# Kernel tuning notes

Measured on AMD Instinct MI355X. Metric: run time of the kernel, lower is better.

Reference implementation:

```python
import jax, jax.numpy as jnp
import numpy as np

B, F, D = 16384, 32, 64
EPS = 1e-5


def layer_norm(x, g, b):
    m = x.mean(-1, keepdims=True)
    v = ((x - m) ** 2).mean(-1, keepdims=True)
    return (x - m) / jnp.sqrt(v + EPS) * g + b


def setup_inputs() -> dict:
    key = jax.random.key(0)
    ks = jax.random.split(key, 24)
    IN = F * D

    def w(k, shape, fan_in):
        return jax.random.normal(k, shape, dtype=jnp.float32) / np.sqrt(fan_in)

    return {
        "x": jax.random.normal(ks[0], (B, F, D), dtype=jnp.float32),
        # StaticGRN (mask branch): Linear(IN,D) -> ELU -> Linear(D,F); skip Linear(IN,F); GateAndNorm(F)
        "mw1": w(ks[1], (IN, D), IN), "mb1": jnp.zeros((D,), jnp.float32),
        "mw2": w(ks[2], (D, F), D), "mb2": jnp.zeros((F,), jnp.float32),
        "mlw": w(ks[3], (IN, F), IN), "mlb": jnp.zeros((F,), jnp.float32),
        "mgw": w(ks[4], (F, F), F), "mgb": jnp.zeros((F,), jnp.float32),
        "mlw2": w(ks[5], (F, F), F), "mlb2": jnp.zeros((F,), jnp.float32),
        "mgamma": jnp.ones((F,), jnp.float32), "mbeta": jnp.zeros((F,), jnp.float32),
        # Per-feature GRNNoContext params, stacked over F (batched small GEMMs)
        "w1": w(ks[6], (F, D, D), D), "b1": jnp.zeros((F, D), jnp.float32),
        "w2": w(ks[7], (F, D, D), D), "b2": jnp.zeros((F, D), jnp.float32),
        "gw": w(ks[8], (F, D, D), D), "gb": jnp.zeros((F, D), jnp.float32),
        "lw": w(ks[9], (F, D, D), D), "lb": jnp.zeros((F, D), jnp.float32),
        "gamma": jnp.ones((F, D), jnp.float32), "beta": jnp.zeros((F, D), jnp.float32),
    }


def reference(x, mw1, mb1, mw2, mb2, mlw, mlb, mgw, mgb, mlw2, mlb2, mgamma, mbeta,
              w1, b1, w2, b2, gw, gb, lw, lb, gamma, beta):
    b, f, d = x.shape
    flat = x.reshape(b, f * d)
    # StaticGRN mask branch (dropout is 0.0 -> identity)
    h = jax.nn.elu(flat @ mw1 + mb1) @ mw2 + mb2          # [B,F]
    res = flat @ mlw + mlb                                 # [B,F] skip path
    pre = jax.nn.sigmoid(h @ mgw + mgb) * (h @ mlw2 + mlb2) + res
    mask = jax.nn.softmax(layer_norm(pre, mgamma, mbeta), axis=-1)[:, None, :]  # [B,1,F]
    # Per-feature GRNs, batched over the feature axis
    hh = jax.nn.elu(jnp.einsum('bfd,fde->bfe', x, w1) + b1)
    hh = jnp.einsum('bfd,fde->bfe', hh, w2) + b2
    gate = jax.nn.sigmoid(jnp.einsum('bfd,fde->bfe', hh, gw) + gb)
    lin = jnp.einsum('bfd,fde->bfe', hh, lw) + lb
    vecs = layer_norm(gate * lin + x, gamma, beta)         # [B,F,D]
    out = jnp.einsum('bof,bfd->bod', mask, vecs)[:, 0, :]  # [B,D]
    return out, mask
```

## Files before the change

### kernel.cpp

```cpp
#include <hip/hip_runtime.h>
#include <hip/hip_bf16.h>
#include <math.h>

#define NB 16384
#define NF 32
#define ND 64
#define NIN 2048

typedef __attribute__((ext_vector_type(8))) short fragA;
typedef __attribute__((ext_vector_type(4))) float fragC;

#define MFMA(a, b, c) __builtin_amdgcn_mfma_f32_16x16x32_bf16((a), (b), (c), 0, 0, 0)

__device__ __forceinline__ short f2bf(float f) {
    union { float f; unsigned u; } v; v.f = f;
    return (short)((v.u + 0x7fffu + ((v.u >> 16) & 1u)) >> 16);
}
__device__ __forceinline__ fragA cvt8(const float* p) {
    const float4 a = *(const float4*)p;
    const float4 b = *(const float4*)(p + 4);
    union { __hip_bfloat162 h[4]; fragA f; } u;
    u.h[0] = __float22bfloat162_rn(make_float2(a.x, a.y));
    u.h[1] = __float22bfloat162_rn(make_float2(a.z, a.w));
    u.h[2] = __float22bfloat162_rn(make_float2(b.x, b.y));
    u.h[3] = __float22bfloat162_rn(make_float2(b.z, b.w));
    return u.f;
}

__global__ __launch_bounds__(256) void prep_kernel(
    const float* __restrict__ w1, const float* __restrict__ w2,
    const float* __restrict__ gw, const float* __restrict__ lw,
    const float* __restrict__ mw1, const float* __restrict__ mlw,
    const float* __restrict__ mw2, const float* __restrict__ mgw,
    const float* __restrict__ mlw2,
    short* __restrict__ wsout)
{
    int F = blockIdx.x * 256 + threadIdx.x;
    fragA o;
    if (F < 65536) {
        int mat = F >> 14;
        int f   = (F >> 9) & 31;
        int nt  = (F >> 7) & 3;
        int s   = (F >> 6) & 1;
        int l   = F & 63;
        const float* src = (mat == 0 ? w1 : mat == 1 ? w2 : mat == 2 ? gw : lw)
                           + (size_t)f * 4096;
        int n  = nt * 16 + (l & 15);
        int k0 = s * 32 + ((l >> 4) << 3);
#pragma unroll
        for (int j = 0; j < 8; ++j) o[j] = f2bf(src[(k0 + j) * 64 + n]);
    } else if (F < 90112) {
        int G  = F - 65536;
        int f  = G / 768;
        int r  = G - f * 768;
        int nt = r >> 7;
        int s  = (r >> 6) & 1;
        int l  = r & 63;
        int n  = nt * 16 + (l & 15);
        int k0 = f * 64 + s * 32 + ((l >> 4) << 3);
        if (n < 64) {
#pragma unroll
            for (int j = 0; j < 8; ++j) o[j] = f2bf(mw1[(size_t)(k0 + j) * 64 + n]);
        } else {
#pragma unroll
            for (int j = 0; j < 8; ++j) o[j] = f2bf(mlw[(size_t)(k0 + j) * 32 + (n - 64)]);
        }
    } else {
        int G2 = F - 90112;
        if (G2 < 256) {
            int nt = G2 >> 7, s = (G2 >> 6) & 1, l = G2 & 63;
            int n = nt * 16 + (l & 15);
            int k0 = s * 32 + ((l >> 4) << 3);
#pragma unroll
            for (int j = 0; j < 8; ++j) o[j] = f2bf(mw2[(k0 + j) * 32 + n]);
        } else {
            int G3 = G2 - 256;
            const float* src = (G3 < 128) ? mgw : mlw2;
            G3 &= 127;
            int nt = G3 >> 6, l = G3 & 63;
            int n = nt * 16 + (l & 15);
            int k0 = (l >> 4) << 3;
#pragma unroll
            for (int j = 0; j < 8; ++j) o[j] = f2bf(src[(k0 + j) * 32 + n]);
        }
    }
    ((fragA*)wsout)[F] = o;
}

__global__ __launch_bounds__(256, 4) void fused_kernel(
    const float* __restrict__ x,
    const short* __restrict__ wfrag, const short* __restrict__ mwfrag,
    const short* __restrict__ swfrag,
    const float* __restrict__ mb1, const float* __restrict__ mb2,
    const float* __restrict__ mlb, const float* __restrict__ mgb,
    const float* __restrict__ mlb2,
    const float* __restrict__ mgamma, const float* __restrict__ mbeta,
    const float* __restrict__ b1, const float* __restrict__ b2,
    const float* __restrict__ gb, const float* __restrict__ lb,
    const float* __restrict__ gamma, const float* __restrict__ beta,
    float* __restrict__ mask_out, float* __restrict__ out)
{
    __shared__ float smem[8960];
    float* redS  = smem;
    float* gS    = smem;
    float* lS    = smem + 768;
    float* hS1   = smem + 1552;
    float* resS  = smem + 2640;
    float* h2S   = smem + 3216;
    float* outS  = smem + 4352;
    float* maskS = smem + 8448;

    const int tid = threadIdx.x;
    const int w = tid >> 6, l = tid & 63;
    const int row0 = blockIdx.x * 16;
    const int m = l & 15, q = l >> 4;

    const fragA* wf  = (const fragA*)wfrag;
    const fragA* mwf = (const fragA*)mwfrag;
    const fragA* swf = (const fragA*)swfrag;

    for (int i = tid; i < 1552; i += 256) redS[i] = 0.f;
    __syncthreads();

    fragC acc[6];
#pragma unroll
    for (int nt = 0; nt < 6; ++nt) acc[nt] = (fragC){0.f, 0.f, 0.f, 0.f};

    const float* xpm = x + (size_t)(row0 + m) * NIN + q * 8;
    for (int fi = 0; fi < 8; ++fi) {
        int f = w * 8 + fi;
        const float* xp = xpm + f * ND;
        fragA a0 = cvt8(xp), a1 = cvt8(xp + 32);
        const size_t fb = (size_t)f * 768 + l;
#pragma unroll
        for (int nt = 0; nt < 6; ++nt) {
            acc[nt] = MFMA(a0, mwf[fb + nt * 128], acc[nt]);
            acc[nt] = MFMA(a1, mwf[fb + nt * 128 + 64], acc[nt]);
        }
    }
#pragma unroll
    for (int nt = 0; nt < 6; ++nt)
#pragma unroll
        for (int rg = 0; rg < 4; ++rg)
            atomicAdd(&redS[(q * 4 + rg) * 97 + nt * 16 + m], acc[nt][rg]);
    __syncthreads();

    {
        int r = tid & 15, cb = tid >> 4;
#pragma unroll
        for (int i = 0; i < 6; ++i) {
            int c = cb + i * 16;
            float s = redS[r * 97 + c];
            if (c < 64) {
                float v = s + mb1[c];
                hS1[r * 68 + c] = v > 0.f ? v : expm1f(v);
            } else {
                resS[r * 36 + (c - 64)] = s + mlb[c - 64];
            }
        }
    }
    __syncthreads();

    if (w < 2) {
        const float* ap = hS1 + m * 68 + q * 8;
        fragA a0 = cvt8(ap), a1 = cvt8(ap + 32);
        fragC c = {0.f, 0.f, 0.f, 0.f};
        c = MFMA(a0, swf[w * 128 + l], c);
        c = MFMA(a1, swf[w * 128 + 64 + l], c);
        float bv = mb2[w * 16 + m];
#pragma unroll
        for (int rg = 0; rg < 4; ++rg)
            h2S[(q * 4 + rg) * 36 + w * 16 + m] = c[rg] + bv;
    }
    __syncthreads();

    {
        int ntc = w & 1;
        int isl = w >> 1;
        fragA a = cvt8(h2S + m * 36 + q * 8);
        fragC c = {0.f, 0.f, 0.f, 0.f};
        c = MFMA(a, swf[256 + isl * 128 + ntc * 64 + l], c);
        float* dst = isl ? lS : gS;
#pragma unroll
        for (int rg = 0; rg < 4; ++rg)
            dst[(q * 4 + rg) * 36 + ntc * 16 + m] = c[rg];
    }
    __syncthreads();

    if (w == 0) {
        int r2 = l >> 2, c0 = (l & 3) * 8;
        float pre[8];
#pragma unroll
        for (int i = 0; i < 8; ++i) {
            int c = c0 + i;
            float gg = gS[r2 * 36 + c] + mgb[c];
            float ll = lS[r2 * 36 + c] + mlb2[c];
            pre[i] = ll / (1.f + expf(-gg)) + resS[r2 * 36 + c];
        }
        float s1 = 0.f;
#pragma unroll
        for (int i = 0; i < 8; ++i) s1 += pre[i];
        s1 += __shfl_xor(s1, 1); s1 += __shfl_xor(s1, 2);
        float mean = s1 * (1.f / 32.f);
        float s2 = 0.f;
#pragma unroll
        for (int i = 0; i < 8; ++i) { float d = pre[i] - mean; s2 += d * d; }
        s2 += __shfl_xor(s2, 1); s2 += __shfl_xor(s2, 2);
        float inv = rsqrtf(s2 * (1.f / 32.f) + 1e-5f);
        float ln[8]; float mx = -3.4e38f;
#pragma unroll
        for (int i = 0; i < 8; ++i) {
            ln[i] = (pre[i] - mean) * inv * mgamma[c0 + i] + mbeta[c0 + i];
            mx = fmaxf(mx, ln[i]);
        }
        mx = fmaxf(mx, __shfl_xor(mx, 1));
        mx = fmaxf(mx, __shfl_xor(mx, 2));
        float ssum = 0.f;
#pragma unroll
        for (int i = 0; i < 8; ++i) { ln[i] = expf(ln[i] - mx); ssum += ln[i]; }
        ssum += __shfl_xor(ssum, 1); ssum += __shfl_xor(ssum, 2);
        float rs = 1.f / ssum;
        float* mo = mask_out + (size_t)(row0 + r2) * 32 + c0;
        *(float4*)mo       = (float4){ln[0] * rs, ln[1] * rs, ln[2] * rs, ln[3] * rs};
        *(float4*)(mo + 4) = (float4){ln[4] * rs, ln[5] * rs, ln[6] * rs, ln[7] * rs};
#pragma unroll
        for (int i = 0; i < 8; ++i) maskS[r2 * 32 + c0 + i] = ln[i] * rs;
    }
    __syncthreads();

    float* hW = smem + w * 1088;

    fragC oac[4];
#pragma unroll
    for (int nt = 0; nt < 4; ++nt) oac[nt] = (fragC){0.f, 0.f, 0.f, 0.f};

    for (int fi = 0; fi < 8; ++fi) {
        int f = w * 8 + fi;
        float xres[4][4];
#pragma unroll
        for (int rg = 0; rg < 4; ++rg)
#pragma unroll
            for (int nt = 0; nt < 4; ++nt)
                xres[rg][nt] = x[(size_t)(row0 + q * 4 + rg) * NIN + f * ND + nt * 16 + m];
        float b1v[4], b2v[4], gbv[4], lbv[4], gmv[4], btv[4];
#pragma unroll
        for (int nt = 0; nt < 4; ++nt) {
            int c = f * 64 + nt * 16 + m;
            b1v[nt] = b1[c]; b2v[nt] = b2[c]; gbv[nt] = gb[c];
            lbv[nt] = lb[c]; gmv[nt] = gamma[c]; btv[nt] = beta[c];
        }
        float mk[4];
#pragma unroll
        for (int rg = 0; rg < 4; ++rg) mk[rg] = maskS[(q * 4 + rg) * 32 + f];

        {
            const float* xp = xpm + f * ND;
            fragA a0 = cvt8(xp), a1 = cvt8(xp + 32);
            const size_t base = (size_t)f * 512 + l;
#pragma unroll
            for (int nt = 0; nt < 4; ++nt) {
                fragC c = {0.f, 0.f, 0.f, 0.f};
                c = MFMA(a0, wf[base + nt * 128], c);
                c = MFMA(a1, wf[base + nt * 128 + 64], c);
                int col = nt * 16 + m;
#pragma unroll
                for (int rg = 0; rg < 4; ++rg) {
                    float v = c[rg] + b1v[nt];
                    hW[(q * 4 + rg) * 68 + col] = v > 0.f ? v : expm1f(v);
                }
            }
        }
        {
            const float* ap = hW + m * 68 + q * 8;
            fragA a0 = cvt8(ap), a1 = cvt8(ap + 32);
            const size_t base = ((size_t)(NF + f)) * 512 + l;
            fragC cc[4];
#pragma unroll
            for (int nt = 0; nt < 4; ++nt) {
                fragC c = {0.f, 0.f, 0.f, 0.f};
                c = MFMA(a0, wf[base + nt * 128], c);
                c = MFMA(a1, wf[base + nt * 128 + 64], c);
                cc[nt] = c;
            }
#pragma unroll
            for (int nt = 0; nt < 4; ++nt) {
                int col = nt * 16 + m;
#pragma unroll
                for (int rg = 0; rg < 4; ++rg)
                    hW[(q * 4 + rg) * 68 + col] = cc[nt][rg] + b2v[nt];
            }
        }
        {
            const float* ap = hW + m * 68 + q * 8;
            fragA a0 = cvt8(ap), a1 = cvt8(ap + 32);
            const size_t baseg = ((size_t)(2 * NF + f)) * 512 + l;
            const size_t basel = ((size_t)(3 * NF + f)) * 512 + l;
            fragC ga[4], la[4];
#pragma unroll
            for (int nt = 0; nt < 4; ++nt) {
                fragC g = {0.f, 0.f, 0.f, 0.f}, li = {0.f, 0.f, 0.f, 0.f};
                g  = MFMA(a0, wf[baseg + nt * 128], g);
                g  = MFMA(a1, wf[baseg + nt * 128 + 64], g);
                li = MFMA(a0, wf[basel + nt * 128], li);
                li = MFMA(a1, wf[basel + nt * 128 + 64], li);
                ga[nt] = g; la[nt] = li;
            }
#pragma unroll
            for (int rg = 0; rg < 4; ++rg) {
                float val[4];
#pragma unroll
                for (int nt = 0; nt < 4; ++nt) {
                    float gg = ga[nt][rg] + gbv[nt];
                    float ll = la[nt][rg] + lbv[nt];
                    val[nt] = ll / (1.f + expf(-gg)) + xres[rg][nt];
                }
                float s1 = val[0] + val[1] + val[2] + val[3];
                s1 += __shfl_xor(s1, 1); s1 += __shfl_xor(s1, 2);
                s1 += __shfl_xor(s1, 4); s1 += __shfl_xor(s1, 8);
                float mean = s1 * (1.f / 64.f);
                float s2 = 0.f;
#pragma unroll
                for (int nt = 0; nt < 4; ++nt) { float d = val[nt] - mean; s2 += d * d; }
                s2 += __shfl_xor(s2, 1); s2 += __shfl_xor(s2, 2);
                s2 += __shfl_xor(s2, 4); s2 += __shfl_xor(s2, 8);
                float inv = rsqrtf(s2 * (1.f / 64.f) + 1e-5f);
#pragma unroll
                for (int nt = 0; nt < 4; ++nt) {
                    float vec = (val[nt] - mean) * inv * gmv[nt] + btv[nt];
                    oac[nt][rg] += mk[rg] * vec;
                }
            }
        }
    }

#pragma unroll
    for (int nt = 0; nt < 4; ++nt)
#pragma unroll
        for (int rg = 0; rg < 4; ++rg)
            outS[w * 1024 + (q * 4 + rg) * 64 + nt * 16 + m] = oac[nt][rg];
    __syncthreads();
    {
        int t4 = tid * 4;
        int r = t4 >> 6, c = t4 & 63;
        float v[4];
#pragma unroll
        for (int j = 0; j < 4; ++j) {
            v[j] = outS[r * 64 + c + j] + outS[1024 + r * 64 + c + j]
                 + outS[2048 + r * 64 + c + j] + outS[3072 + r * 64 + c + j];
        }
        *(float4*)(out + (size_t)(row0 + r) * 64 + c) = (float4){v[0], v[1], v[2], v[3]};
    }
}

extern "C" void kernel_launch(void* const* d_in, const int* in_sizes, int n_in,
                              void* d_out, int out_size, void* d_ws, size_t ws_size,
                              hipStream_t stream) {
    const float* x      = (const float*)d_in[0];
    const float* mw1    = (const float*)d_in[1];
    const float* mb1    = (const float*)d_in[2];
    const float* mw2    = (const float*)d_in[3];
    const float* mb2    = (const float*)d_in[4];
    const float* mlw    = (const float*)d_in[5];
    const float* mlb    = (const float*)d_in[6];
    const float* mgw    = (const float*)d_in[7];
    const float* mgb    = (const float*)d_in[8];
    const float* mlw2   = (const float*)d_in[9];
    const float* mlb2   = (const float*)d_in[10];
    const float* mgamma = (const float*)d_in[11];
    const float* mbeta  = (const float*)d_in[12];
    const float* w1     = (const float*)d_in[13];
    const float* b1     = (const float*)d_in[14];
    const float* w2     = (const float*)d_in[15];
    const float* b2     = (const float*)d_in[16];
    const float* gw     = (const float*)d_in[17];
    const float* gb     = (const float*)d_in[18];
    const float* lw     = (const float*)d_in[19];
    const float* lb     = (const float*)d_in[20];
    const float* gamma  = (const float*)d_in[21];
    const float* beta   = (const float*)d_in[22];

    float* out  = (float*)d_out;
    float* mask = out + (size_t)NB * 64;

    short* wfrag  = (short*)d_ws;
    short* mwfrag = wfrag + (size_t)65536 * 8;
    short* swfrag = wfrag + (size_t)90112 * 8;

    hipLaunchKernelGGL(prep_kernel, dim3(354), dim3(256), 0, stream,
                       w1, w2, gw, lw, mw1, mlw, mw2, mgw, mlw2, wfrag);
    hipLaunchKernelGGL(fused_kernel, dim3(NB / 16), dim3(256), 0, stream,
                       x, wfrag, mwfrag, swfrag,
                       mb1, mb2, mlb, mgb, mlb2, mgamma, mbeta,
                       b1, b2, gb, lb, gamma, beta,
                       mask, out);
}
```

Before: 345.8 us.

## Interleave two features per wave in per-feature GRN loop and use fast intrinsics

Each wave now processes two features at once, with separate LDS scratch buffers, and interleaves their independent MFMA chains to expose more instruction-level parallelism and hide MFMA and LDS latency. Exact expf, expm1f and division are replaced by __expf and __fdividef in the ELU, gate and softmax. The residual x loads and bias loads move to the point of use instead of being prefetched per feature. The LDS layout is reorganised so the output buffer aliases the start of shared memory, with an extra barrier before it is written. This raises register pressure and LDS use, which may reduce occupancy, and slightly lowers numerical accuracy.

New measurement: 381.8 us. 10.4% more time.

```diff
diff --git a/kernel.cpp b/kernel.cpp
--- a/kernel.cpp
+++ b/kernel.cpp
@@ -25,6 +25,12 @@
     u.h[2] = __float22bfloat162_rn(make_float2(b.x, b.y));
     u.h[3] = __float22bfloat162_rn(make_float2(b.z, b.w));
     return u.f;
+}
+__device__ __forceinline__ float fast_elu(float v) {
+    return v > 0.f ? v : (__expf(v) - 1.f);
+}
+__device__ __forceinline__ float fast_gate(float ll, float gg) {
+    return __fdividef(ll, 1.f + __expf(-gg));
 }
 
 __global__ __launch_bounds__(256) void prep_kernel(
@@ -100,15 +106,15 @@
     const float* __restrict__ gamma, const float* __restrict__ beta,
     float* __restrict__ mask_out, float* __restrict__ out)
 {
-    __shared__ float smem[8960];
+    __shared__ float smem[9216];
     float* redS  = smem;
     float* gS    = smem;
     float* lS    = smem + 768;
     float* hS1   = smem + 1552;
     float* resS  = smem + 2640;
     float* h2S   = smem + 3216;
-    float* outS  = smem + 4352;
-    float* maskS = smem + 8448;
+    float* outS  = smem;
+    float* maskS = smem + 8704;
 
     const int tid = threadIdx.x;
     const int w = tid >> 6, l = tid & 63;
@@ -152,8 +158,7 @@
             int c = cb + i * 16;
             float s = redS[r * 97 + c];
             if (c < 64) {
-                float v = s + mb1[c];
-                hS1[r * 68 + c] = v > 0.f ? v : expm1f(v);
+                hS1[r * 68 + c] = fast_elu(s + mb1[c]);
             } else {
                 resS[r * 36 + (c - 64)] = s + mlb[c - 64];
             }
@@ -195,7 +200,7 @@
             int c = c0 + i;
             float gg = gS[r2 * 36 + c] + mgb[c];
             float ll = lS[r2 * 36 + c] + mlb2[c];
-            pre[i] = ll / (1.f + expf(-gg)) + resS[r2 * 36 + c];
+            pre[i] = fast_gate(ll, gg) + resS[r2 * 36 + c];
         }
         float s1 = 0.f;
 #pragma unroll
@@ -217,9 +222,9 @@
         mx = fmaxf(mx, __shfl_xor(mx, 2));
         float ssum = 0.f;
 #pragma unroll
-        for (int i = 0; i < 8; ++i) { ln[i] = expf(ln[i] - mx); ssum += ln[i]; }
+        for (int i = 0; i < 8; ++i) { ln[i] = __expf(ln[i] - mx); ssum += ln[i]; }
         ssum += __shfl_xor(ssum, 1); ssum += __shfl_xor(ssum, 2);
-        float rs = 1.f / ssum;
+        float rs = __fdividef(1.f, ssum);
         float* mo = mask_out + (size_t)(row0 + r2) * 32 + c0;
         *(float4*)mo       = (float4){ln[0] * rs, ln[1] * rs, ln[2] * rs, ln[3] * rs};
         *(float4*)(mo + 4) = (float4){ln[4] * rs, ln[5] * rs, ln[6] * rs, ln[7] * rs};
@@ -228,111 +233,141 @@
     }
     __syncthreads();
 
-    float* hW = smem + w * 1088;
+    float* hWa = smem + w * 2176;
+    float* hWb = smem + w * 2176 + 1088;
 
     fragC oac[4];
 #pragma unroll
     for (int nt = 0; nt < 4; ++nt) oac[nt] = (fragC){0.f, 0.f, 0.f, 0.f};
 
-    for (int fi = 0; fi < 8; ++fi) {
-        int f = w * 8 + fi;
-        float xres[4][4];
-#pragma unroll
-        for (int rg = 0; rg < 4; ++rg)
-#pragma unroll
-            for (int nt = 0; nt < 4; ++nt)
-                xres[rg][nt] = x[(size_t)(row0 + q * 4 + rg) * NIN + f * ND + nt * 16 + m];
-        float b1v[4], b2v[4], gbv[4], lbv[4], gmv[4], btv[4];
-#pragma unroll
-        for (int nt = 0; nt < 4; ++nt) {
-            int c = f * 64 + nt * 16 + m;
-            b1v[nt] = b1[c]; b2v[nt] = b2[c]; gbv[nt] = gb[c];
-            lbv[nt] = lb[c]; gmv[nt] = gamma[c]; btv[nt] = beta[c];
-        }
-        float mk[4];
-#pragma unroll
-        for (int rg = 0; rg < 4; ++rg) mk[rg] = maskS[(q * 4 + rg) * 32 + f];
+    for (int fi = 0; fi < 4; ++fi) {
+        const int fA = w * 8 + fi;
+        const int fB = fA + 4;
 
         {
-            const float* xp = xpm + f * ND;
-            fragA a0 = cvt8(xp), a1 = cvt8(xp + 32);
-            const size_t base = (size_t)f * 512 + l;
+            const float* xpA = xpm + fA * ND;
+            const float* xpB = xpm + fB * ND;
+            fragA a0A = cvt8(xpA), a1A = cvt8(xpA + 32);
+            fragA a0B = cvt8(xpB), a1B = cvt8(xpB + 32);
+            const size_t bA = (size_t)fA * 512 + l;
+            const size_t bB = (size_t)fB * 512 + l;
 #pragma unroll
             for (int nt = 0; nt < 4; ++nt) {
-                fragC c = {0.f, 0.f, 0.f, 0.f};
-                c = MFMA(a0, wf[base + nt * 128], c);
-                c = MFMA(a1, wf[base + nt * 128 + 64], c);
+                fragC cA = {0.f, 0.f, 0.f, 0.f}, cB = {0.f, 0.f, 0.f, 0.f};
+                cA = MFMA(a0A, wf[bA + nt * 128], cA);
+                cB = MFMA(a0B, wf[bB + nt * 128], cB);
+                cA = MFMA(a1A, wf[bA + nt * 128 + 64], cA);
+                cB = MFMA(a1B, wf[bB + nt * 128 + 64], cB);
                 int col = nt * 16 + m;
+                float bvA = b1[fA * 64 + col], bvB = b1[fB * 64 + col];
 #pragma unroll
                 for (int rg = 0; rg < 4; ++rg) {
-                    float v = c[rg] + b1v[nt];
-                    hW[(q * 4 + rg) * 68 + col] = v > 0.f ? v : expm1f(v);
+                    hWa[(q * 4 + rg) * 68 + col] = fast_elu(cA[rg] + bvA);
+                    hWb[(q * 4 + rg) * 68 + col] = fast_elu(cB[rg] + bvB);
                 }
             }
         }
         {
-            const float* ap = hW + m * 68 + q * 8;
-            fragA a0 = cvt8(ap), a1 = cvt8(ap + 32);
-            const size_t base = ((size_t)(NF + f)) * 512 + l;
-            fragC cc[4];
+            const float* apA = hWa + m * 68 + q * 8;
+            const float* apB = hWb + m * 68 + q * 8;
+            fragA a0A = cvt8(apA), a1A = cvt8(apA + 32);
+            fragA a0B = cvt8(apB), a1B = cvt8(apB + 32);
+            const size_t bA = ((size_t)(NF + fA)) * 512 + l;
+            const size_t bB = ((size_t)(NF + fB)) * 512 + l;
+            fragC ccA[4], ccB[4];
 #pragma unroll
             for (int nt = 0; nt < 4; ++nt) {
-                fragC c = {0.f, 0.f, 0.f, 0.f};
-                c = MFMA(a0, wf[base + nt * 128], c);
-                c = MFMA(a1, wf[base + nt * 128 + 64], c);
-                cc[nt] = c;
+                fragC cA = {0.f, 0.f, 0.f, 0.f}, cB = {0.f, 0.f, 0.f, 0.f};
+                cA = MFMA(a0A, wf[bA + nt * 128], cA);
+                cB = MFMA(a0B, wf[bB + nt * 128], cB);
+                cA = MFMA(a1A, wf[bA + nt * 128 + 64], cA);
+                cB = MFMA(a1B, wf[bB + nt * 128 + 64], cB);
+                ccA[nt] = cA; ccB[nt] = cB;
             }
 #pragma unroll
             for (int nt = 0; nt < 4; ++nt) {
                 int col = nt * 16 + m;
-#pragma unroll
-                for (int rg = 0; rg < 4; ++rg)
-                    hW[(q * 4 + rg) * 68 + col] = cc[nt][rg] + b2v[nt];
+                float bvA = b2[fA * 64 + col], bvB = b2[fB * 64 + col];
+#pragma unroll
+                for (int rg = 0; rg < 4; ++rg) {
+                    hWa[(q * 4 + rg) * 68 + col] = ccA[nt][rg] + bvA;
+                    hWb[(q * 4 + rg) * 68 + col] = ccB[nt][rg] + bvB;
+                }
             }
         }
         {
-            const float* ap = hW + m * 68 + q * 8;
-            fragA a0 = cvt8(ap), a1 = cvt8(ap + 32);
-            const size_t baseg = ((size_t)(2 * NF + f)) * 512 + l;
-            const size_t basel = ((size_t)(3 * NF + f)) * 512 + l;
-            fragC ga[4], la[4];
+            const float* apA = hWa + m * 68 + q * 8;
+            const float* apB = hWb + m * 68 + q * 8;
+            fragA a0A = cvt8(apA), a1A = cvt8(apA + 32);
+            fragA a0B = cvt8(apB), a1B = cvt8(apB + 32);
+            const size_t bgA = ((size_t)(2 * NF + fA)) * 512 + l;
+            const size_t blA = ((size_t)(3 * NF + fA)) * 512 + l;
+            const size_t bgB = ((size_t)(2 * NF + fB)) * 512 + l;
+            const size_t blB = ((size_t)(3 * NF + fB)) * 512 + l;
+            fragC gaA[4], laA[4], gaB[4], laB[4];
 #pragma unroll
             for (int nt = 0; nt < 4; ++nt) {
                 fragC g = {0.f, 0.f, 0.f, 0.f}, li = {0.f, 0.f, 0.f, 0.f};
-                g  = MFMA(a0, wf[baseg + nt * 128], g);
-                g  = MFMA(a1, wf[baseg + nt * 128 + 64], g);
-                li = MFMA(a0, wf[basel + nt * 128], li);
-                li = MFMA(a1, wf[basel + nt * 128 + 64], li);
-                ga[nt] = g; la[nt] = li;
-            }
-#pragma unroll
-            for (int rg = 0; rg < 4; ++rg) {
-                float val[4];
+                g  = MFMA(a0A, wf[bgA + nt * 128], g);
+                g  = MFMA(a1A, wf[bgA + nt * 128 + 64], g);
+                li = MFMA(a0A, wf[blA + nt * 128], li);
+                li = MFMA(a1A, wf[blA + nt * 128 + 64], li);
+                gaA[nt] = g; laA[nt] = li;
+            }
+#pragma unroll
+            for (int nt = 0; nt < 4; ++nt) {
+                fragC g = {0.f, 0.f, 0.f, 0.f}, li = {0.f, 0.f, 0.f, 0.f};
+                g  = MFMA(a0B, wf[bgB + nt * 128], g);
+                g  = MFMA(a1B, wf[bgB + nt * 128 + 64], g);
+                li = MFMA(a0B, wf[blB + nt * 128], li);
+                li = MFMA(a1B, wf[blB + nt * 128 + 64], li);
+                gaB[nt] = g; laB[nt] = li;
+            }
+#pragma unroll
+            for (int ch = 0; ch < 2; ++ch) {
+                const int f = ch ? fB : fA;
+                fragC* ga = ch ? gaB : gaA;
+                fragC* la = ch ? laB : laA;
+                float gbv[4], lbv[4], gmv[4], btv[4];
 #pragma unroll
                 for (int nt = 0; nt < 4; ++nt) {
-                    float gg = ga[nt][rg] + gbv[nt];
-                    float ll = la[nt][rg] + lbv[nt];
-                    val[nt] = ll / (1.f + expf(-gg)) + xres[rg][nt];
+                    int c = f * 64 + nt * 16 + m;
+                    gbv[nt] = gb[c]; lbv[nt] = lb[c];
+                    gmv[nt] = gamma[c]; btv[nt] = beta[c];
                 }
-                float s1 = val[0] + val[1] + val[2] + val[3];
-                s1 += __shfl_xor(s1, 1); s1 += __shfl_xor(s1, 2);
-                s1 += __shfl_xor(s1, 4); s1 += __shfl_xor(s1, 8);
-                float mean = s1 * (1.f / 64.f);
-                float s2 = 0.f;
-#pragma unroll
-                for (int nt = 0; nt < 4; ++nt) { float d = val[nt] - mean; s2 += d * d; }
-                s2 += __shfl_xor(s2, 1); s2 += __shfl_xor(s2, 2);
-                s2 += __shfl_xor(s2, 4); s2 += __shfl_xor(s2, 8);
-                float inv = rsqrtf(s2 * (1.f / 64.f) + 1e-5f);
-#pragma unroll
-                for (int nt = 0; nt < 4; ++nt) {
-                    float vec = (val[nt] - mean) * inv * gmv[nt] + btv[nt];
-                    oac[nt][rg] += mk[rg] * vec;
+#pragma unroll
+                for (int rg = 0; rg < 4; ++rg) {
+                    int row = q * 4 + rg;
+                    float mk = maskS[row * 32 + f];
+                    float val[4];
+#pragma unroll
+                    for (int nt = 0; nt < 4; ++nt) {
+                        float gg = ga[nt][rg] + gbv[nt];
+                        float ll = la[nt][rg] + lbv[nt];
+                        float resid = x[(size_t)(row0 + row) * NIN + f * ND + nt * 16 + m];
+                        val[nt] = fast_gate(ll, gg) + resid;
+                    }
+                    float s1 = val[0] + val[1] + val[2] + val[3];
+                    s1 += __shfl_xor(s1, 1); s1 += __shfl_xor(s1, 2);
+                    s1 += __shfl_xor(s1, 4); s1 += __shfl_xor(s1, 8);
+                    float mean = s1 * (1.f / 64.f);
+                    float s2 = 0.f;
+#pragma unroll
+                    for (int nt = 0; nt < 4; ++nt) { float d = val[nt] - mean; s2 += d * d; }
+                    s2 += __shfl_xor(s2, 1); s2 += __shfl_xor(s2, 2);
+                    s2 += __shfl_xor(s2, 4); s2 += __shfl_xor(s2, 8);
+                    float inv = rsqrtf(s2 * (1.f / 64.f) + 1e-5f);
+#pragma unroll
+                    for (int nt = 0; nt < 4; ++nt) {
+                        float vec = (val[nt] - mean) * inv * gmv[nt] + btv[nt];
+                        oac[nt][rg] += mk * vec;
+                    }
                 }
             }
         }
     }
 
+    __syncthreads();
 #pragma unroll
     for (int nt = 0; nt < 4; ++nt)
 #pragma unroll
```
